# Kernel optimization log

Hardware: AMD Instinct MI355X
Metric: run time of the kernel (lower is better)

## Reference

```python
import jax, jax.numpy as jnp
import numpy as np
import math


def _alibi_slopes(num_heads: int) -> np.ndarray:
    def power_of_2(n):
        ratio = 2.0 ** (-8.0 / n)
        return np.array([ratio ** i for i in range(n)], dtype=np.float32)
    if math.log2(num_heads).is_integer():
        return power_of_2(num_heads)
    nearest = 2 ** math.floor(math.log2(num_heads))
    return np.concatenate([power_of_2(nearest), power_of_2(2 * nearest)[::2][: num_heads - nearest]])


def _rmsnorm(x, w, eps=1e-6):
    var = jnp.mean(x * x, axis=-1, keepdims=True)
    return x * jax.lax.rsqrt(var + eps) * w


def setup_inputs() -> dict:
    key = jax.random.key(0)
    ks = jax.random.split(key, 6)
    B, S, M = 2, 2048, 1024
    H, KV, D = 16, 4, 64
    s = 0.02
    return {
        "features": jax.random.normal(ks[0], (B, S, M), jnp.float32),
        "wq": jax.random.normal(ks[1], (H * D, M), jnp.float32) * s,
        "wk": jax.random.normal(ks[2], (KV * D, M), jnp.float32) * s,
        "wv": jax.random.normal(ks[3], (KV * D, M), jnp.float32) * s,
        "wo": jax.random.normal(ks[4], (M, H * D), jnp.float32) * s,
        "q_norm_w": jnp.ones((H * D,), jnp.float32),
        "k_norm_w": jnp.ones((KV * D,), jnp.float32),
        "num_heads": 16,
        "num_kv_heads": 4,
        "head_dim": 64,
        "sliding_window": 512,
    }


def reference(features, wq, wk, wv, wo, q_norm_w, k_norm_w, num_heads, num_kv_heads, head_dim, sliding_window):
    B, S, M = features.shape
    H, KV, D = num_heads, num_kv_heads, head_dim
    kv_rep = H // KV

    q = features @ wq.T                                   # [B,S,H*D]
    k = features @ wk.T                                   # [B,S,KV*D]
    v = features @ wv.T                                   # [B,S,KV*D]
    q = _rmsnorm(q, q_norm_w)
    k = _rmsnorm(k, k_norm_w)

    q = q.reshape(B, S, H, D).transpose(0, 2, 1, 3)       # [B,H,S,D]
    k = k.reshape(B, S, KV, D)
    v = v.reshape(B, S, KV, D)
    k = jnp.repeat(k, kv_rep, axis=2).transpose(0, 2, 1, 3)  # [B,H,S,D]
    v = jnp.repeat(v, kv_rep, axis=2).transpose(0, 2, 1, 3)

    pos = jnp.arange(S)
    rel = pos[None, :] - pos[:, None]                     # [S,S], j - i
    slopes = jnp.asarray(_alibi_slopes(H))
    bias = slopes[:, None, None] * rel.astype(features.dtype)  # [H,S,S]
    invalid = (rel > 0) | (rel < -sliding_window)         # causal + left window
    bias = jnp.where(invalid[None], -jnp.inf, bias)

    scores = jnp.einsum("bhqd,bhkd->bhqk", q, k) / math.sqrt(D)
    attn = jax.nn.softmax(scores + bias[None], axis=-1)
    out = jnp.einsum("bhqk,bhkd->bhqd", attn, v)
    out = out.transpose(0, 2, 1, 3).reshape(B, S, H * D)
    return out @ wo.T
```

## Files before the change

kernel.cpp:

```cpp
#include <hip/hip_runtime.h>
#include <hip/hip_bf16.h>

typedef __bf16 bf16_t;
typedef bf16_t bf16x8 __attribute__((ext_vector_type(8)));
typedef bf16_t bf16x4 __attribute__((ext_vector_type(4)));
typedef float  f32x4  __attribute__((ext_vector_type(4)));
typedef float  f32x16 __attribute__((ext_vector_type(16)));

__device__ __forceinline__ f32x4 mfma16(bf16x8 a, bf16x8 b, f32x4 c) {
  return __builtin_amdgcn_mfma_f32_16x16x32_bf16(a, b, c, 0, 0, 0);
}
__device__ __forceinline__ f32x16 mfma32(bf16x8 a, bf16x8 b, f32x16 c) {
  return __builtin_amdgcn_mfma_f32_32x32x16_bf16(a, b, c, 0, 0, 0);
}

__global__ __launch_bounds__(256) void cast_all_k(const float* __restrict__ f,
                                                  const float* __restrict__ wq,
                                                  const float* __restrict__ wk,
                                                  const float* __restrict__ wv,
                                                  const float* __restrict__ wo,
                                                  bf16_t* __restrict__ Xbf,
                                                  bf16_t* __restrict__ Wqkv,
                                                  bf16_t* __restrict__ Wo) {
  int i = blockIdx.x * 256 + threadIdx.x;
  const float* src; bf16_t* dst; int off;
  if (i < 1048576)      { src = f;  dst = Xbf;                 off = 0; }
  else if (i < 1310720) { src = wq; dst = Wqkv;                off = 1048576; }
  else if (i < 1376256) { src = wk; dst = Wqkv + 1024 * 1024;  off = 1310720; }
  else if (i < 1441792) { src = wv; dst = Wqkv + 1280 * 1024;  off = 1376256; }
  else if (i < 1703936) { src = wo; dst = Wo;                  off = 1441792; }
  else return;
  int j = i - off;
  float4 v = reinterpret_cast<const float4*>(src)[j];
  bf16x4 o = { (bf16_t)v.x, (bf16_t)v.y, (bf16_t)v.z, (bf16_t)v.w };
  reinterpret_cast<bf16x4*>(dst)[j] = o;
}

template<int BM, typename CT>
__global__ __launch_bounds__(256) void gemm_bt(const bf16_t* __restrict__ A,
                                               const bf16_t* __restrict__ B,
                                               CT* __restrict__ C,
                                               int M, int N, int K) {
  constexpr int MR = BM / 32;
  __shared__ __align__(16) unsigned short sA[2][BM * 64];
  __shared__ __align__(16) unsigned short sB[2][128 * 64];
  const int tid = threadIdx.x;
  const int lane = tid & 63;
  const int wid = tid >> 6;
  const int wm = wid >> 1, wn = wid & 1;
  const int lr = lane & 15, lg = lane >> 4;
  const int m0 = blockIdx.y * BM, n0 = blockIdx.x * 128;

  f32x4 acc[MR][4] = {};

  auto STAGE = [&](int buf, int k0) {
#pragma unroll
    for (int r = 0; r < BM / 32; ++r) {
      int e = r * 2048 + tid * 8;
      int row = e >> 6;
      int cc = ((e >> 3) & 7) ^ (row & 7);
      const bf16_t* ga = A + (size_t)(m0 + row) * K + k0 + cc * 8;
      __builtin_amdgcn_global_load_lds(
          (const __attribute__((address_space(1))) void*)ga,
          (__attribute__((address_space(3))) void*)(&sA[buf][r * 2048 + wid * 512]), 16, 0, 0);
    }
#pragma unroll
    for (int r = 0; r < 4; ++r) {
      int e = r * 2048 + tid * 8;
      int row = e >> 6;
      int cc = ((e >> 3) & 7) ^ (row & 7);
      const bf16_t* gb = B + (size_t)(n0 + row) * K + k0 + cc * 8;
      __builtin_amdgcn_global_load_lds(
          (const __attribute__((address_space(1))) void*)gb,
          (__attribute__((address_space(3))) void*)(&sB[buf][r * 2048 + wid * 512]), 16, 0, 0);
    }
  };

  const int nt = K >> 6;
  STAGE(0, 0);
  if (nt > 1) STAGE(1, 64);
  for (int t = 0; t < nt; ++t) {
    if (t < nt - 1) asm volatile("s_waitcnt vmcnt(6)" ::: "memory");
    else            asm volatile("s_waitcnt vmcnt(0)" ::: "memory");
    asm volatile("s_barrier" ::: "memory");
    __builtin_amdgcn_sched_barrier(0);
    const int cur = t & 1;
#pragma unroll
    for (int ks = 0; ks < 2; ++ks) {
      bf16x8 afr[MR], bfr[4];
#pragma unroll
      for (int m = 0; m < MR; ++m) {
        int row = wm * (BM / 2) + m * 16 + lr;
        int sc = (ks * 4 + lg) ^ (row & 7);
        afr[m] = *reinterpret_cast<const bf16x8*>(&sA[cur][row * 64 + sc * 8]);
      }
#pragma unroll
      for (int n = 0; n < 4; ++n) {
        int row = wn * 64 + n * 16 + lr;
        int sc = (ks * 4 + lg) ^ (row & 7);
        bfr[n] = *reinterpret_cast<const bf16x8*>(&sB[cur][row * 64 + sc * 8]);
      }
#pragma unroll
      for (int m = 0; m < MR; ++m)
#pragma unroll
        for (int n = 0; n < 4; ++n)
          acc[m][n] = mfma16(afr[m], bfr[n], acc[m][n]);
    }
    asm volatile("s_barrier" ::: "memory");
    if (t + 2 < nt) STAGE(cur, (t + 2) << 6);
  }
#pragma unroll
  for (int m = 0; m < MR; ++m)
#pragma unroll
    for (int n = 0; n < 4; ++n) {
      int row = m0 + wm * (BM / 2) + m * 16 + lg * 4;
      int col = n0 + wn * 64 + n * 16 + lr;
#pragma unroll
      for (int r2 = 0; r2 < 4; ++r2)
        C[(size_t)(row + r2) * N + col] = (CT)acc[m][n][r2];
    }
}

__global__ __launch_bounds__(256) void norm_trans_k(const bf16_t* __restrict__ qkv,
                                                    const float* __restrict__ qw,
                                                    const float* __restrict__ kw,
                                                    bf16_t* __restrict__ qn,
                                                    bf16_t* __restrict__ kn,
                                                    bf16_t* __restrict__ vt) {
  __shared__ float t[64][65];
  const int tid = threadIdx.x;
  if (blockIdx.x < 4096) {
    const int row = blockIdx.x;
    const int b = row >> 11, s = row & 2047;
    const bf16_t* rp = qkv + (size_t)row * 1536;
    bf16x4 qb = *reinterpret_cast<const bf16x4*>(rp + tid * 4);
    float q0 = (float)qb[0], q1 = (float)qb[1], q2 = (float)qb[2], q3 = (float)qb[3];
    float kv1 = (float)rp[1024 + tid];
    float sq = q0 * q0 + q1 * q1 + q2 * q2 + q3 * q3;
    float sk = kv1 * kv1;
#pragma unroll
    for (int d = 1; d < 64; d <<= 1) {
      sq += __shfl_xor(sq, d, 64);
      sk += __shfl_xor(sk, d, 64);
    }
    if ((tid & 63) == 0) { t[0][tid >> 6] = sq; t[0][4 + (tid >> 6)] = sk; }
    __syncthreads();
    sq = t[0][0] + t[0][1] + t[0][2] + t[0][3];
    sk = t[0][4] + t[0][5] + t[0][6] + t[0][7];
    const float rq = rsqrtf(sq * (1.0f / 1024.0f) + 1e-6f);
    const float rk = rsqrtf(sk * (1.0f / 256.0f) + 1e-6f);
    float4 w4 = *reinterpret_cast<const float4*>(qw + tid * 4);
    const int c = tid * 4, hh = c >> 6, d0 = c & 63;
    bf16x4 o = { (bf16_t)(q0 * rq * w4.x), (bf16_t)(q1 * rq * w4.y),
                 (bf16_t)(q2 * rq * w4.z), (bf16_t)(q3 * rq * w4.w) };
    *reinterpret_cast<bf16x4*>(qn + ((size_t)((b * 16 + hh) * 2048 + s)) * 64 + d0) = o;
    const int kvh = tid >> 6, dk = tid & 63;
    kn[((size_t)((b * 4 + kvh) * 2048 + s)) * 64 + dk] = (bf16_t)(kv1 * rk * kw[tid]);
  } else {
    const int idx = blockIdx.x - 4096;
    const int s0 = (idx & 31) * 64;
    const int bkv = idx >> 5;
    const int b = bkv >> 2, kv = bkv & 3;
    const int r = tid >> 2, cg = (tid & 3) * 16;
    const bf16_t* src = qkv + (size_t)(b * 2048 + s0 + r) * 1536 + 1280 + kv * 64 + cg;
    bf16x8 v0 = *reinterpret_cast<const bf16x8*>(src);
    bf16x8 v1 = *reinterpret_cast<const bf16x8*>(src + 8);
#pragma unroll
    for (int j = 0; j < 8; ++j) {
      t[r][cg + j] = (float)v0[j];
      t[r][cg + 8 + j] = (float)v1[j];
    }
    __syncthreads();
    const int dl = tid >> 4;
    const int sl = (tid & 15) * 4;
    const int kt = (s0 >> 5) + (sl >> 5);
    const int p0 = (sl & 16) + ((sl >> 2) & 1) * 8 + ((sl >> 3) & 1) * 4;
#pragma unroll
    for (int p = 0; p < 4; ++p) {
      const int d = dl + p * 16;
      bf16x4 o = { (bf16_t)t[sl + 0][d], (bf16_t)t[sl + 1][d],
                   (bf16_t)t[sl + 2][d], (bf16_t)t[sl + 3][d] };
      *reinterpret_cast<bf16x4*>(vt + (size_t)bkv * 131072 + (size_t)kt * 2048 + d * 32 + p0) = o;
    }
  }
}

__global__ __launch_bounds__(256, 4) void attn_k(const bf16_t* __restrict__ qn,
                                                 const bf16_t* __restrict__ kn,
                                                 const bf16_t* __restrict__ vt,
                                                 bf16_t* __restrict__ ao) {
  constexpr int S = 2048, D = 64, H = 16, KV = 4, WIN = 512;
  const int bkv = blockIdx.x;
  const int b = bkv >> 2, kv = bkv & 3;
  const int h = kv * 4 + blockIdx.z;
  const int wid = threadIdx.x >> 6;
  const int pair = wid >> 1;
  const int kh = wid & 1;
  const int qblk = blockIdx.y * 2 + pair;
  const int lane = threadIdx.x & 63;
  const int c = lane & 31;
  const int hi = lane >> 5;
  const int qbase = qblk * 32;
  const int q = qbase + c;

  __shared__ float lsh[2][2][32];
  __shared__ float accbuf[2][64][33];

  const bf16_t* qp = qn + ((size_t)(b * H + h) * S + q) * D + hi * 8;
  bf16x8 qf[4];
#pragma unroll
  for (int cd = 0; cd < 4; ++cd) qf[cd] = *reinterpret_cast<const bf16x8*>(qp + cd * 16);

  const bf16_t* kb = kn + (size_t)bkv * S * D;
  const bf16_t* vb = vt + (size_t)bkv * 131072;

  const float L2E = 1.4426950408889634f;
  const float MSTAT = 8.0f * L2E;
  const float c1 = L2E / 8.0f;
  const float c2 = exp2f(-0.5f * (float)h) * L2E;

  f32x16 acc0 = {}, acc1 = {};
  float l_run = 0.0f;

  const int ktTop = qbase >> 5;
  const int kt0 = (qbase >= WIN) ? ((qbase - WIN) >> 5) : 0;

  for (int kt = ktTop - kh; kt >= kt0; kt -= 2) {
    const int k0 = kt << 5;
    const bf16_t* kp = kb + (((size_t)k0 + c) << 6) + hi * 8;
    f32x16 sfa = {};
    __builtin_amdgcn_s_setprio(1);
#pragma unroll
    for (int cd = 0; cd < 4; ++cd) {
      bf16x8 kf = *reinterpret_cast<const bf16x8*>(kp + cd * 16);
      sfa = mfma32(kf, qf[cd], sfa);
    }
    __builtin_amdgcn_s_setprio(0);
    const bool edge = (kt == ktTop) | (k0 + WIN < qbase + 32);
    const float bbm = fmaf(c2, (float)(k0 + 4 * hi - q), -MSTAT);
    float rs = 0.0f;
    unsigned w[8];
#pragma unroll
    for (int i = 0; i < 8; ++i) {
      float e2[2];
#pragma unroll
      for (int j = 0; j < 2; ++j) {
        const int r = 2 * i + j;
        const float koff = (float)((r & 3) + 8 * (r >> 2));
        if (edge) {
          const int rel = k0 + (int)koff + 4 * hi - q;
          float tv = fmaf(sfa[r], c1, fmaf((float)rel, c2, -MSTAT));
          tv = (rel > 0 || rel < -WIN) ? -3.0e38f : tv;
          e2[j] = exp2f(tv);
        } else {
          e2[j] = exp2f(fmaf(sfa[r], c1, fmaf(koff, c2, bbm)));
        }
      }
      rs += e2[0] + e2[1];
      union { bf16_t hh[2]; unsigned u; } pk;
      pk.hh[0] = (bf16_t)e2[0]; pk.hh[1] = (bf16_t)e2[1];
      w[i] = pk.u;
    }
    rs += __shfl_xor(rs, 32, 64);
    l_run += rs;
    union { unsigned u[4]; bf16x8 v; } pa0, pa1;
    pa0.u[0] = w[0]; pa0.u[1] = w[1]; pa0.u[2] = w[2]; pa0.u[3] = w[3];
    pa1.u[0] = w[4]; pa1.u[1] = w[5]; pa1.u[2] = w[6]; pa1.u[3] = w[7];
    const bf16_t* vp = vb + ((size_t)kt << 11) + c * 32 + hi * 8;
    bf16x8 v00 = *reinterpret_cast<const bf16x8*>(vp);
    bf16x8 v01 = *reinterpret_cast<const bf16x8*>(vp + 16);
    bf16x8 v10 = *reinterpret_cast<const bf16x8*>(vp + 1024);
    bf16x8 v11 = *reinterpret_cast<const bf16x8*>(vp + 1024 + 16);
    __builtin_amdgcn_s_setprio(1);
    acc0 = mfma32(pa0.v, v00, acc0);
    acc0 = mfma32(pa1.v, v01, acc0);
    acc1 = mfma32(pa0.v, v10, acc1);
    acc1 = mfma32(pa1.v, v11, acc1);
    __builtin_amdgcn_s_setprio(0);
  }

  lsh[pair][kh][c] = l_run;
  if (kh == 1) {
#pragma unroll
    for (int r = 0; r < 16; ++r) {
      accbuf[pair][lane][r] = acc0[r];
      accbuf[pair][lane][r + 16] = acc1[r];
    }
  }
  __syncthreads();
  if (kh == 0) {
    const float l_tot = l_run + lsh[pair][1][c];
#pragma unroll
    for (int r = 0; r < 16; ++r) {
      acc0[r] += accbuf[pair][lane][r];
      acc1[r] += accbuf[pair][lane][r + 16];
    }
#pragma unroll
    for (int r = 0; r < 16; ++r) {
      const int qi = (r & 3) + 8 * (r >> 2) + 4 * hi;
      const float lr = __shfl(l_tot, qi, 64);
      const float inv = 1.0f / lr;
      bf16_t* op = ao + ((size_t)(b * S + qbase + qi)) * 1024 + h * 64 + c;
      op[0]  = (bf16_t)(acc0[r] * inv);
      op[32] = (bf16_t)(acc1[r] * inv);
    }
  }
}

extern "C" void kernel_launch(void* const* d_in, const int* in_sizes, int n_in,
                              void* d_out, int out_size, void* d_ws, size_t ws_size,
                              hipStream_t stream) {
  const float* features = (const float*)d_in[0];
  const float* wq = (const float*)d_in[1];
  const float* wk = (const float*)d_in[2];
  const float* wv = (const float*)d_in[3];
  const float* wo = (const float*)d_in[4];
  const float* qw = (const float*)d_in[5];
  const float* kw = (const float*)d_in[6];
  float* out = (float*)d_out;

  bf16_t* Xbf  = (bf16_t*)d_ws;
  bf16_t* Wqkv = Xbf + 4096 * 1024;
  bf16_t* Wo   = Wqkv + 1536 * 1024;
  bf16_t* QKVr = Wo + 1024 * 1024;
  bf16_t* Qn   = QKVr + 4096 * 1536;
  bf16_t* Kn   = Qn + 2 * 16 * 2048 * 64;
  bf16_t* Vt   = Kn + 2 * 4 * 2048 * 64;
  bf16_t* Ao   = Vt + 2 * 4 * 64 * 2048;

  cast_all_k<<<6656, 256, 0, stream>>>(features, wq, wk, wv, wo, Xbf, Wqkv, Wo);
  gemm_bt<64, bf16_t><<<dim3(12, 64), 256, 0, stream>>>(Xbf, Wqkv, QKVr, 4096, 1536, 1024);
  norm_trans_k<<<4352, 256, 0, stream>>>(QKVr, qw, kw, Qn, Kn, Vt);
  attn_k<<<dim3(8, 32, 4), 256, 0, stream>>>(Qn, Kn, Vt, Ao);
  gemm_bt<64, float><<<dim3(8, 64), 256, 0, stream>>>(Ao, Wo, out, 4096, 1024, 1024);
}
```

Baseline: 86.60 us.

## Process two key tiles per iteration and defer row-sum reduction to epilogue

The attention loop now issues the QK^T MFMAs for two consecutive key tiles before running the softmax and PV step on each. Each wave handles pairs of tiles, stepping by four. The per-tile cross-half shuffle of the row sum is removed; partial sums per half are stored to shared memory and added in the epilogue. Launch bounds drop from 4 to 2 blocks per CU to leave more registers for the extra live score tile, at the cost of lower occupancy.

Result: no change. 87.01 us (+0.5%).

```diff
diff --git a/kernel.cpp b/kernel.cpp
--- a/kernel.cpp
+++ b/kernel.cpp
@@ -185,7 +185,7 @@
   }
 }
 
-__global__ __launch_bounds__(256, 4) void attn_k(const bf16_t* __restrict__ qn,
+__global__ __launch_bounds__(256, 2) void attn_k(const bf16_t* __restrict__ qn,
                                                  const bf16_t* __restrict__ kn,
                                                  const bf16_t* __restrict__ vt,
                                                  bf16_t* __restrict__ ao) {
@@ -203,7 +203,7 @@
   const int qbase = qblk * 32;
   const int q = qbase + c;
 
-  __shared__ float lsh[2][2][32];
+  __shared__ float lsh[2][2][2][32];
   __shared__ float accbuf[2][64][33];
 
   const bf16_t* qp = qn + ((size_t)(b * H + h) * S + q) * D + hi * 8;
@@ -225,18 +225,9 @@
   const int ktTop = qbase >> 5;
   const int kt0 = (qbase >= WIN) ? ((qbase - WIN) >> 5) : 0;
 
-  for (int kt = ktTop - kh; kt >= kt0; kt -= 2) {
+  auto PROC = [&](int kt, bool isTop, const f32x16& sfa) {
     const int k0 = kt << 5;
-    const bf16_t* kp = kb + (((size_t)k0 + c) << 6) + hi * 8;
-    f32x16 sfa = {};
-    __builtin_amdgcn_s_setprio(1);
-#pragma unroll
-    for (int cd = 0; cd < 4; ++cd) {
-      bf16x8 kf = *reinterpret_cast<const bf16x8*>(kp + cd * 16);
-      sfa = mfma32(kf, qf[cd], sfa);
-    }
-    __builtin_amdgcn_s_setprio(0);
-    const bool edge = (kt == ktTop) | (k0 + WIN < qbase + 32);
+    const bool edge = isTop | (k0 + WIN < qbase + 32);
     const float bbm = fmaf(c2, (float)(k0 + 4 * hi - q), -MSTAT);
     float rs = 0.0f;
     unsigned w[8];
@@ -261,7 +252,6 @@
       pk.hh[0] = (bf16_t)e2[0]; pk.hh[1] = (bf16_t)e2[1];
       w[i] = pk.u;
     }
-    rs += __shfl_xor(rs, 32, 64);
     l_run += rs;
     union { unsigned u[4]; bf16x8 v; } pa0, pa1;
     pa0.u[0] = w[0]; pa0.u[1] = w[1]; pa0.u[2] = w[2]; pa0.u[3] = w[3];
@@ -277,9 +267,36 @@
     acc1 = mfma32(pa0.v, v10, acc1);
     acc1 = mfma32(pa1.v, v11, acc1);
     __builtin_amdgcn_s_setprio(0);
-  }
-
-  lsh[pair][kh][c] = l_run;
+  };
+
+  for (int kt = ktTop - 2 * kh; kt >= kt0; kt -= 4) {
+    const int ktB = kt - 1;
+    const bool hasB = (ktB >= kt0);
+    const bf16_t* kpA = kb + (((size_t)(kt << 5) + c) << 6) + hi * 8;
+    f32x16 sfaA = {};
+    __builtin_amdgcn_s_setprio(1);
+#pragma unroll
+    for (int cd = 0; cd < 4; ++cd) {
+      bf16x8 kf = *reinterpret_cast<const bf16x8*>(kpA + cd * 16);
+      sfaA = mfma32(kf, qf[cd], sfaA);
+    }
+    __builtin_amdgcn_s_setprio(0);
+    f32x16 sfaB = {};
+    if (hasB) {
+      const bf16_t* kpB = kb + (((size_t)(ktB << 5) + c) << 6) + hi * 8;
+      __builtin_amdgcn_s_setprio(1);
+#pragma unroll
+      for (int cd = 0; cd < 4; ++cd) {
+        bf16x8 kf = *reinterpret_cast<const bf16x8*>(kpB + cd * 16);
+        sfaB = mfma32(kf, qf[cd], sfaB);
+      }
+      __builtin_amdgcn_s_setprio(0);
+    }
+    PROC(kt, kt == ktTop, sfaA);
+    if (hasB) PROC(ktB, false, sfaB);
+  }
+
+  lsh[pair][kh][hi][c] = l_run;
   if (kh == 1) {
 #pragma unroll
     for (int r = 0; r < 16; ++r) {
@@ -289,7 +306,8 @@
   }
   __syncthreads();
   if (kh == 0) {
-    const float l_tot = l_run + lsh[pair][1][c];
+    const float l_tot = lsh[pair][0][0][c] + lsh[pair][0][1][c]
+                      + lsh[pair][1][0][c] + lsh[pair][1][1][c];
 #pragma unroll
     for (int r = 0; r < 16; ++r) {
       acc0[r] += accbuf[pair][lane][r];
```
